# Optimization experiments

Hardware: AMD Instinct MI355X
Metric: run time of the kernel (lower is better)

The kernel has to match this reference:

```python
import jax, jax.numpy as jnp
import numpy as np

VIEW, SEQ, HID = 8, 2048, 1024
ATT = HID // VIEW  # 128


def setup_inputs() -> dict:
    key = jax.random.key(0)
    ks = jax.random.split(key, 12)
    std = 0.02
    return {
        "q": jax.random.normal(ks[0], (VIEW, SEQ, HID), jnp.float32),
        "k": jax.random.normal(ks[1], (VIEW, SEQ, HID), jnp.float32),
        "v": jax.random.normal(ks[2], (VIEW, SEQ, HID), jnp.float32),
        "attn_bias": jax.random.normal(ks[3], (VIEW, SEQ, SEQ), jnp.float32) * std,
        "wq": jax.random.normal(ks[4], (HID, ATT), jnp.float32) * std,
        "bq": jnp.zeros((ATT,), jnp.float32),
        "wk": jax.random.normal(ks[5], (HID, ATT), jnp.float32) * std,
        "bk": jnp.zeros((ATT,), jnp.float32),
        "wv": jax.random.normal(ks[6], (HID, ATT), jnp.float32) * std,
        "bv": jnp.zeros((ATT,), jnp.float32),
        "wo": jax.random.normal(ks[7], (VIEW * ATT, HID), jnp.float32) * std,
        "bo": jnp.zeros((HID,), jnp.float32),
    }


def reference(q, k, v, attn_bias, wq, bq, wk, bk, wv, bv, wo, bo):
    att = wq.shape[1]
    scale = att ** (-0.5)
    qh = (q @ wq + bq) * scale            # [V, S, A]
    kh = k @ wk + bk                      # [V, S, A]
    vh = v @ wv + bv                      # [V, S, A]
    scores = jnp.einsum("vqa,vka->vqk", qh, kh)   # [V, S, S]
    attn = jax.nn.softmax(scores, axis=2)
    # NOTE: source adds the bias AFTER softmax; dropout p=0 (identity).
    attn = attn + attn_bias
    x = jnp.einsum("vqk,vka->vqa", attn, vh)      # [V, S, A]
    vdim, sdim, adim = x.shape
    x = jnp.transpose(x, (1, 0, 2)).reshape(sdim, vdim * adim)  # [S, V*A]
    return x @ wo + bo                    # [S, HID]
```

## Files before the change

kernel.cpp:

```cpp
#include <hip/hip_runtime.h>
#include <math.h>

#define VIEWS 8
#define SEQ 2048
#define HID 1024
#define ATT 128
#define QSCALE 0.08838834764831845f

typedef __attribute__((ext_vector_type(8))) short short8;
typedef __attribute__((ext_vector_type(4))) float f32x4;

__device__ __forceinline__ unsigned short f2bf(float f) {
  union { float f; unsigned u; } a; a.f = f;
  unsigned r = a.u + 0x7FFF + ((a.u >> 16) & 1);
  return (unsigned short)(r >> 16);
}

__global__ __launch_bounds__(256)
void transpose_cvt_f32_bf16(const float* __restrict__ in,
                            unsigned short* __restrict__ out, int R, int C) {
  __shared__ alignas(16) unsigned short T[64][72];
  const int tid = threadIdx.x;
  const int r0 = blockIdx.y * 64, c0 = blockIdx.x * 64;
  const int tr = tid >> 2, tc = (tid & 3) * 16;
#pragma unroll
  for (int u = 0; u < 4; ++u) {
    float4 t = *(const float4*)&in[(size_t)(r0 + tr) * C + c0 + tc + u * 4];
    T[tc + u * 4 + 0][tr] = f2bf(t.x);
    T[tc + u * 4 + 1][tr] = f2bf(t.y);
    T[tc + u * 4 + 2][tr] = f2bf(t.z);
    T[tc + u * 4 + 3][tr] = f2bf(t.w);
  }
  __syncthreads();
  const int oc = tid >> 2, orr = (tid & 3) * 16;
#pragma unroll
  for (int u = 0; u < 2; ++u)
    *(short8*)&out[(size_t)(c0 + oc) * R + r0 + orr + u * 8] =
        *(const short8*)&T[oc][orr + u * 8];
}

__global__ __launch_bounds__(256)
void transpose_qkvw(const float* __restrict__ wq, const float* __restrict__ wk,
                    const float* __restrict__ wv, unsigned short* __restrict__ oq,
                    unsigned short* __restrict__ ok, unsigned short* __restrict__ ov) {
  __shared__ alignas(16) unsigned short T[64][72];
  const int z = blockIdx.z;
  const float* in = (z == 0) ? wq : (z == 1) ? wk : wv;
  unsigned short* out = (z == 0) ? oq : (z == 1) ? ok : ov;
  const int R = HID, C = ATT;
  const int tid = threadIdx.x;
  const int r0 = blockIdx.y * 64, c0 = blockIdx.x * 64;
  const int tr = tid >> 2, tc = (tid & 3) * 16;
#pragma unroll
  for (int u = 0; u < 4; ++u) {
    float4 t = *(const float4*)&in[(size_t)(r0 + tr) * C + c0 + tc + u * 4];
    T[tc + u * 4 + 0][tr] = f2bf(t.x);
    T[tc + u * 4 + 1][tr] = f2bf(t.y);
    T[tc + u * 4 + 2][tr] = f2bf(t.z);
    T[tc + u * 4 + 3][tr] = f2bf(t.w);
  }
  __syncthreads();
  const int oc = tid >> 2, orr = (tid & 3) * 16;
#pragma unroll
  for (int u = 0; u < 2; ++u)
    *(short8*)&out[(size_t)(c0 + oc) * R + r0 + orr + u * 8] =
        *(const short8*)&T[oc][orr + u * 8];
}

__global__ __launch_bounds__(256)
void qkv_proj(const float* __restrict__ q, const float* __restrict__ k,
              const float* __restrict__ v, const unsigned short* __restrict__ wqT,
              const unsigned short* __restrict__ wkT,
              const unsigned short* __restrict__ wvT,
              const float* __restrict__ bq, const float* __restrict__ bk,
              const float* __restrict__ bv, unsigned short* __restrict__ qh,
              unsigned short* __restrict__ kh, unsigned short* __restrict__ vhT) {
  __shared__ alignas(16) unsigned short As[64][72];
  __shared__ alignas(16) unsigned short Bs[128][72];
  const int z = blockIdx.z;
  const float* A = (z == 0) ? q : (z == 1) ? k : v;
  const unsigned short* B = (z == 0) ? wqT : (z == 1) ? wkT : wvT;
  const float* bias = (z == 0) ? bq : (z == 1) ? bk : bv;
  const float scale = (z == 0) ? QSCALE : 1.0f;
  const int tid = threadIdx.x;
  const int m0 = blockIdx.x * 64;
  const int w = tid >> 6, lane = tid & 63;
  const int l16 = lane & 15, quad = lane >> 4;
  const int ar = tid >> 2, ac = (tid & 3) * 16;
  const int br = tid >> 1, bc = (tid & 1) * 32;

  f32x4 acc[8];
#pragma unroll
  for (int i = 0; i < 8; ++i) acc[i] = (f32x4)0.f;

  for (int k0 = 0; k0 < HID; k0 += 64) {
    __syncthreads();
    {
      const float* src = &A[(size_t)(m0 + ar) * HID + k0 + ac];
      unsigned short tmp[16];
#pragma unroll
      for (int u = 0; u < 4; ++u) {
        float4 t = *(const float4*)&src[u * 4];
        tmp[u * 4 + 0] = f2bf(t.x); tmp[u * 4 + 1] = f2bf(t.y);
        tmp[u * 4 + 2] = f2bf(t.z); tmp[u * 4 + 3] = f2bf(t.w);
      }
      *(short8*)&As[ar][ac]     = *(short8*)&tmp[0];
      *(short8*)&As[ar][ac + 8] = *(short8*)&tmp[8];
    }
    {
      const unsigned short* src = &B[(size_t)br * HID + k0 + bc];
#pragma unroll
      for (int u = 0; u < 4; ++u)
        *(short8*)&Bs[br][bc + u * 8] = *(const short8*)&src[u * 8];
    }
    __syncthreads();
#pragma unroll
    for (int ks = 0; ks < 2; ++ks) {
      short8 af = *(const short8*)&As[w * 16 + l16][ks * 32 + quad * 8];
#pragma unroll
      for (int nt = 0; nt < 8; ++nt) {
        short8 bf = *(const short8*)&Bs[nt * 16 + l16][ks * 32 + quad * 8];
        acc[nt] = __builtin_amdgcn_mfma_f32_16x16x32_bf16(af, bf, acc[nt], 0, 0, 0);
      }
    }
  }
  if (z < 2) {
    unsigned short* outp = (z == 0) ? qh : kh;
#pragma unroll
    for (int nt = 0; nt < 8; ++nt) {
      const int col = nt * 16 + l16;
      const float bvv = bias[col];
#pragma unroll
      for (int reg = 0; reg < 4; ++reg) {
        const int row = m0 + w * 16 + quad * 4 + reg;
        outp[(size_t)row * ATT + col] = f2bf((acc[nt][reg] + bvv) * scale);
      }
    }
  } else {
    const int gr = m0 + w * 16 + quad * 4;
    const int vi = gr >> 11, s = gr & (SEQ - 1);
#pragma unroll
    for (int nt = 0; nt < 8; ++nt) {
      const int col = nt * 16 + l16;
      const float bvv = bias[col];
      ushort4 pk;
      pk.x = f2bf(acc[nt][0] + bvv);
      pk.y = f2bf(acc[nt][1] + bvv);
      pk.z = f2bf(acc[nt][2] + bvv);
      pk.w = f2bf(acc[nt][3] + bvv);
      *(ushort4*)&vhT[((size_t)vi * ATT + col) * SEQ + s] = pk;
    }
  }
}

__global__ __launch_bounds__(256, 1)
void flash_fused(const unsigned short* __restrict__ qh,
                 const unsigned short* __restrict__ kh,
                 const unsigned short* __restrict__ vhT,
                 const float* __restrict__ ab,
                 unsigned short* __restrict__ xbf) {
  __shared__ alignas(16) unsigned short Qs[64][136];
  __shared__ alignas(16) unsigned short Ks[2][64][136];
  __shared__ alignas(16) unsigned short VTs[2][128][72];
  __shared__ alignas(16) unsigned short Ps[64][72];
  const int tid = threadIdx.x;
  const int vi = blockIdx.x;
  const int q0 = blockIdx.y * 64;
  const int w = tid >> 6, lane = tid & 63;
  const int l16 = lane & 15, quad = lane >> 4;
  const int wb = w * 16;

  const int kr_ = tid >> 2, kc_ = (tid & 3) * 32;
  const int vr_ = tid >> 1, vc_ = (tid & 1) * 32;
  const unsigned short* kbase = &kh[((size_t)vi * SEQ + kr_) * ATT + kc_];
  const unsigned short* vbase = &vhT[((size_t)vi * ATT + vr_) * SEQ + vc_];

  {
    const int r = tid >> 2, c = (tid & 3) * 32;
    const unsigned short* src = &qh[((size_t)vi * SEQ + q0 + r) * ATT + c];
#pragma unroll
    for (int u = 0; u < 4; ++u)
      *(short8*)&Qs[r][c + u * 8] = *(const short8*)&src[u * 8];
  }

  short8 krg[4], vrg[4];
#pragma unroll
  for (int u = 0; u < 4; ++u) krg[u] = *(const short8*)&kbase[u * 8];
#pragma unroll
  for (int u = 0; u < 4; ++u) vrg[u] = *(const short8*)&vbase[u * 8];

  __syncthreads();
  short8 aF[4];
#pragma unroll
  for (int ks = 0; ks < 4; ++ks)
    aF[ks] = *(const short8*)&Qs[wb + l16][ks * 32 + quad * 8];

  float l_r[4] = {0.f, 0.f, 0.f, 0.f};
  f32x4 o[8], o2[8];
#pragma unroll
  for (int i = 0; i < 8; ++i) { o[i] = (f32x4)0.f; o2[i] = (f32x4)0.f; }

  const float* abrow = &ab[((size_t)vi * SEQ + q0 + wb + l16) * SEQ];

  for (int t = 0; t < SEQ / 64; ++t) {
    const int kt = t * 64;
    const int cur = t & 1;
    float4 abv[4];
    abv[0] = *(const float4*)&abrow[kt + quad * 8];
    abv[1] = *(const float4*)&abrow[kt + quad * 8 + 4];
    abv[2] = *(const float4*)&abrow[kt + 32 + quad * 8];
    abv[3] = *(const float4*)&abrow[kt + 32 + quad * 8 + 4];
#pragma unroll
    for (int u = 0; u < 4; ++u)
      *(short8*)&Ks[cur][kr_][kc_ + u * 8] = krg[u];
#pragma unroll
    for (int u = 0; u < 4; ++u)
      *(short8*)&VTs[cur][vr_][vc_ + u * 8] = vrg[u];
    __syncthreads();
    if (t + 1 < SEQ / 64) {
      const unsigned short* kp = kbase + (size_t)(kt + 64) * ATT;
      const unsigned short* vp = vbase + (kt + 64);
#pragma unroll
      for (int u = 0; u < 4; ++u) krg[u] = *(const short8*)&kp[u * 8];
#pragma unroll
      for (int u = 0; u < 4; ++u) vrg[u] = *(const short8*)&vp[u * 8];
    }
    f32x4 sc[4];
#pragma unroll
    for (int i = 0; i < 4; ++i) sc[i] = (f32x4)0.f;
#pragma unroll
    for (int nt = 0; nt < 4; ++nt) {
#pragma unroll
      for (int ks = 0; ks < 4; ++ks) {
        short8 bF = *(const short8*)&Ks[cur][nt * 16 + l16][ks * 32 + quad * 8];
        sc[nt] = __builtin_amdgcn_mfma_f32_16x16x32_bf16(aF[ks], bF, sc[nt], 0, 0, 0);
      }
    }
#pragma unroll
    for (int nt = 0; nt < 4; ++nt) {
#pragma unroll
      for (int reg = 0; reg < 4; ++reg) {
        float p = __expf(sc[nt][reg]);
        l_r[reg] += p;
        Ps[wb + quad * 4 + reg][nt * 16 + l16] = f2bf(p);
      }
    }
#pragma unroll
    for (int ks = 0; ks < 2; ++ks) {
      short8 pF = *(const short8*)&Ps[wb + l16][ks * 32 + quad * 8];
      short8 bB;
      {
        const float4 u0 = abv[ks * 2], u1 = abv[ks * 2 + 1];
        bB[0] = (short)f2bf(u0.x); bB[1] = (short)f2bf(u0.y);
        bB[2] = (short)f2bf(u0.z); bB[3] = (short)f2bf(u0.w);
        bB[4] = (short)f2bf(u1.x); bB[5] = (short)f2bf(u1.y);
        bB[6] = (short)f2bf(u1.z); bB[7] = (short)f2bf(u1.w);
      }
#pragma unroll
      for (int at = 0; at < 8; ++at) {
        short8 vF = *(const short8*)&VTs[cur][at * 16 + l16][ks * 32 + quad * 8];
        o[at]  = __builtin_amdgcn_mfma_f32_16x16x32_bf16(pF, vF, o[at], 0, 0, 0);
        o2[at] = __builtin_amdgcn_mfma_f32_16x16x32_bf16(bB, vF, o2[at], 0, 0, 0);
      }
    }
  }
  float inv_l[4];
#pragma unroll
  for (int reg = 0; reg < 4; ++reg) {
    float l = l_r[reg];
    l += __shfl_xor(l, 1, 64);
    l += __shfl_xor(l, 2, 64);
    l += __shfl_xor(l, 4, 64);
    l += __shfl_xor(l, 8, 64);
    inv_l[reg] = 1.0f / l;
  }
#pragma unroll
  for (int at = 0; at < 8; ++at) {
    const int col = vi * ATT + at * 16 + l16;
#pragma unroll
    for (int reg = 0; reg < 4; ++reg) {
      const int row = q0 + wb + quad * 4 + reg;
      xbf[(size_t)row * HID + col] = f2bf(o[at][reg] * inv_l[reg] + o2[at][reg]);
    }
  }
}

__global__ __launch_bounds__(256)
void outproj_gemm(const unsigned short* __restrict__ A,
                  const unsigned short* __restrict__ B,
                  const float* __restrict__ bias, float* __restrict__ out) {
  __shared__ alignas(16) unsigned short As[2][64][72];
  __shared__ alignas(16) unsigned short Bs[2][128][72];
  const int tid = threadIdx.x;
  const int m0 = blockIdx.x * 64;
  const int n0 = blockIdx.y * 128;
  const int w = tid >> 6, lane = tid & 63;
  const int l16 = lane & 15, quad = lane >> 4;
  const int ar = tid >> 2, ac = (tid & 3) * 16;
  const int br = tid >> 1, bc = (tid & 1) * 32;
  const unsigned short* abase = &A[(size_t)(m0 + ar) * HID + ac];
  const unsigned short* bbase = &B[(size_t)(n0 + br) * HID + bc];

  f32x4 acc[8];
#pragma unroll
  for (int i = 0; i < 8; ++i) acc[i] = (f32x4)0.f;

  short8 arg0, arg1, brg[4];
  arg0 = *(const short8*)&abase[0];
  arg1 = *(const short8*)&abase[8];
#pragma unroll
  for (int u = 0; u < 4; ++u) brg[u] = *(const short8*)&bbase[u * 8];

  for (int kk = 0; kk < HID / 64; ++kk) {
    const int cur = kk & 1;
    *(short8*)&As[cur][ar][ac]     = arg0;
    *(short8*)&As[cur][ar][ac + 8] = arg1;
#pragma unroll
    for (int u = 0; u < 4; ++u)
      *(short8*)&Bs[cur][br][bc + u * 8] = brg[u];
    __syncthreads();
    if (kk + 1 < HID / 64) {
      const unsigned short* ap = abase + (kk + 1) * 64;
      const unsigned short* bp = bbase + (kk + 1) * 64;
      arg0 = *(const short8*)&ap[0];
      arg1 = *(const short8*)&ap[8];
#pragma unroll
      for (int u = 0; u < 4; ++u) brg[u] = *(const short8*)&bp[u * 8];
    }
#pragma unroll
    for (int ks = 0; ks < 2; ++ks) {
      short8 af = *(const short8*)&As[cur][w * 16 + l16][ks * 32 + quad * 8];
#pragma unroll
      for (int nt = 0; nt < 8; ++nt) {
        short8 bf = *(const short8*)&Bs[cur][nt * 16 + l16][ks * 32 + quad * 8];
        acc[nt] = __builtin_amdgcn_mfma_f32_16x16x32_bf16(af, bf, acc[nt], 0, 0, 0);
      }
    }
  }
#pragma unroll
  for (int nt = 0; nt < 8; ++nt) {
    const int col = n0 + nt * 16 + l16;
    const float bvv = bias[col];
#pragma unroll
    for (int reg = 0; reg < 4; ++reg) {
      const int row = m0 + w * 16 + quad * 4 + reg;
      out[(size_t)row * HID + col] = acc[nt][reg] + bvv;
    }
  }
}

extern "C" void kernel_launch(void* const* d_in, const int* in_sizes, int n_in,
                              void* d_out, int out_size, void* d_ws, size_t ws_size,
                              hipStream_t stream) {
  const float* q   = (const float*)d_in[0];
  const float* k   = (const float*)d_in[1];
  const float* v   = (const float*)d_in[2];
  const float* ab  = (const float*)d_in[3];
  const float* wq  = (const float*)d_in[4];
  const float* bq  = (const float*)d_in[5];
  const float* wk  = (const float*)d_in[6];
  const float* bk  = (const float*)d_in[7];
  const float* wv  = (const float*)d_in[8];
  const float* bv  = (const float*)d_in[9];
  const float* wo  = (const float*)d_in[10];
  const float* bo  = (const float*)d_in[11];
  float* out = (float*)d_out;

  char* ws = (char*)d_ws;
  const size_t PROJ_B = (size_t)VIEWS * SEQ * ATT * 2;
  unsigned short* qh  = (unsigned short*)(ws);
  unsigned short* kh  = (unsigned short*)(ws + PROJ_B);
  unsigned short* vhT = (unsigned short*)(ws + 2 * PROJ_B);
  unsigned short* xbf = (unsigned short*)(ws + 3 * PROJ_B);
  char* wbase = ws + 4 * PROJ_B;
  unsigned short* wqT = (unsigned short*)(wbase);
  unsigned short* wkT = (unsigned short*)(wbase + 262144);
  unsigned short* wvT = (unsigned short*)(wbase + 2 * 262144);
  unsigned short* woT = (unsigned short*)(wbase + 3 * 262144);

  dim3 blk(256);
  transpose_qkvw<<<dim3(2, 16, 3), blk, 0, stream>>>(wq, wk, wv, wqT, wkT, wvT);
  transpose_cvt_f32_bf16<<<dim3(16, 16), blk, 0, stream>>>(wo, woT, HID, HID);
  qkv_proj<<<dim3(256, 1, 3), blk, 0, stream>>>(q, k, v, wqT, wkT, wvT,
                                                bq, bk, bv, qh, kh, vhT);
  flash_fused<<<dim3(VIEWS, SEQ / 64), blk, 0, stream>>>(qh, kh, vhT, ab, xbf);
  outproj_gemm<<<dim3(SEQ / 64, HID / 128), blk, 0, stream>>>(xbf, woT, bo, out);
}
```

Before: 416.7 us.

## Load QKV projection operands directly into MFMA fragments, dropping LDS staging

Rewrites qkv_proj so each wave loads its A rows (fp32, converted to bf16 in registers) and B weight rows straight from global memory into MFMA fragments, removing the shared-memory tiles and both barriers per k-step. Block tile shrinks to 32 rows with waves split 2x2 over M and N, the grid doubles to 512 blocks per projection, and launch bounds request 4 blocks per CU. This trades LDS traffic and sync stalls for redundant global/L2 loads: each A row is now read by two waves and each weight row by many blocks, and the per-lane global access pattern is strided.

```diff
diff --git a/kernel.cpp b/kernel.cpp
--- a/kernel.cpp
+++ b/kernel.cpp
@@ -67,7 +67,7 @@
         *(const short8*)&T[oc][orr + u * 8];
 }
 
-__global__ __launch_bounds__(256)
+__global__ __launch_bounds__(256, 4)
 void qkv_proj(const float* __restrict__ q, const float* __restrict__ k,
               const float* __restrict__ v, const unsigned short* __restrict__ wqT,
               const unsigned short* __restrict__ wkT,
@@ -75,73 +75,70 @@
               const float* __restrict__ bq, const float* __restrict__ bk,
               const float* __restrict__ bv, unsigned short* __restrict__ qh,
               unsigned short* __restrict__ kh, unsigned short* __restrict__ vhT) {
-  __shared__ alignas(16) unsigned short As[64][72];
-  __shared__ alignas(16) unsigned short Bs[128][72];
   const int z = blockIdx.z;
   const float* A = (z == 0) ? q : (z == 1) ? k : v;
   const unsigned short* B = (z == 0) ? wqT : (z == 1) ? wkT : wvT;
   const float* bias = (z == 0) ? bq : (z == 1) ? bk : bv;
   const float scale = (z == 0) ? QSCALE : 1.0f;
   const int tid = threadIdx.x;
-  const int m0 = blockIdx.x * 64;
   const int w = tid >> 6, lane = tid & 63;
   const int l16 = lane & 15, quad = lane >> 4;
-  const int ar = tid >> 2, ac = (tid & 3) * 16;
-  const int br = tid >> 1, bc = (tid & 1) * 32;
-
-  f32x4 acc[8];
-#pragma unroll
-  for (int i = 0; i < 8; ++i) acc[i] = (f32x4)0.f;
-
+  const int mbase = blockIdx.x * 32 + (w & 1) * 16;
+  const int n0 = (w >> 1) * 64;
+
+  const float* arow = &A[(size_t)(mbase + l16) * HID + quad * 8];
+  const unsigned short* bbase = &B[(size_t)(n0 + l16) * HID + quad * 8];
+
+  f32x4 acc[4];
+#pragma unroll
+  for (int i = 0; i < 4; ++i) acc[i] = (f32x4)0.f;
+
+#pragma unroll 2
   for (int k0 = 0; k0 < HID; k0 += 64) {
-    __syncthreads();
-    {
-      const float* src = &A[(size_t)(m0 + ar) * HID + k0 + ac];
-      unsigned short tmp[16];
-#pragma unroll
-      for (int u = 0; u < 4; ++u) {
-        float4 t = *(const float4*)&src[u * 4];
-        tmp[u * 4 + 0] = f2bf(t.x); tmp[u * 4 + 1] = f2bf(t.y);
-        tmp[u * 4 + 2] = f2bf(t.z); tmp[u * 4 + 3] = f2bf(t.w);
-      }
-      *(short8*)&As[ar][ac]     = *(short8*)&tmp[0];
-      *(short8*)&As[ar][ac + 8] = *(short8*)&tmp[8];
-    }
-    {
-      const unsigned short* src = &B[(size_t)br * HID + k0 + bc];
-#pragma unroll
-      for (int u = 0; u < 4; ++u)
-        *(short8*)&Bs[br][bc + u * 8] = *(const short8*)&src[u * 8];
-    }
-    __syncthreads();
-#pragma unroll
-    for (int ks = 0; ks < 2; ++ks) {
-      short8 af = *(const short8*)&As[w * 16 + l16][ks * 32 + quad * 8];
-#pragma unroll
-      for (int nt = 0; nt < 8; ++nt) {
-        short8 bf = *(const short8*)&Bs[nt * 16 + l16][ks * 32 + quad * 8];
-        acc[nt] = __builtin_amdgcn_mfma_f32_16x16x32_bf16(af, bf, acc[nt], 0, 0, 0);
-      }
-    }
-  }
+    const float4 a0 = *(const float4*)&arow[k0];
+    const float4 a1 = *(const float4*)&arow[k0 + 4];
+    const float4 a2 = *(const float4*)&arow[k0 + 32];
+    const float4 a3 = *(const float4*)&arow[k0 + 36];
+    short8 bfr[8];
+#pragma unroll
+    for (int nt = 0; nt < 4; ++nt) {
+      bfr[nt * 2]     = *(const short8*)&bbase[(size_t)nt * 16 * HID + k0];
+      bfr[nt * 2 + 1] = *(const short8*)&bbase[(size_t)nt * 16 * HID + k0 + 32];
+    }
+    short8 af0, af1;
+    af0[0] = (short)f2bf(a0.x); af0[1] = (short)f2bf(a0.y);
+    af0[2] = (short)f2bf(a0.z); af0[3] = (short)f2bf(a0.w);
+    af0[4] = (short)f2bf(a1.x); af0[5] = (short)f2bf(a1.y);
+    af0[6] = (short)f2bf(a1.z); af0[7] = (short)f2bf(a1.w);
+    af1[0] = (short)f2bf(a2.x); af1[1] = (short)f2bf(a2.y);
+    af1[2] = (short)f2bf(a2.z); af1[3] = (short)f2bf(a2.w);
+    af1[4] = (short)f2bf(a3.x); af1[5] = (short)f2bf(a3.y);
+    af1[6] = (short)f2bf(a3.z); af1[7] = (short)f2bf(a3.w);
+#pragma unroll
+    for (int nt = 0; nt < 4; ++nt) {
+      acc[nt] = __builtin_amdgcn_mfma_f32_16x16x32_bf16(af0, bfr[nt * 2],     acc[nt], 0, 0, 0);
+      acc[nt] = __builtin_amdgcn_mfma_f32_16x16x32_bf16(af1, bfr[nt * 2 + 1], acc[nt], 0, 0, 0);
+    }
+  }
+
   if (z < 2) {
     unsigned short* outp = (z == 0) ? qh : kh;
 #pragma unroll
-    for (int nt = 0; nt < 8; ++nt) {
-      const int col = nt * 16 + l16;
+    for (int nt = 0; nt < 4; ++nt) {
+      const int col = n0 + nt * 16 + l16;
       const float bvv = bias[col];
 #pragma unroll
       for (int reg = 0; reg < 4; ++reg) {
-        const int row = m0 + w * 16 + quad * 4 + reg;
+        const int row = mbase + quad * 4 + reg;
         outp[(size_t)row * ATT + col] = f2bf((acc[nt][reg] + bvv) * scale);
       }
     }
   } else {
-    const int gr = m0 + w * 16 + quad * 4;
+    const int gr = mbase + quad * 4;
     const int vi = gr >> 11, s = gr & (SEQ - 1);
 #pragma unroll
-    for (int nt = 0; nt < 8; ++nt) {
-      const int col = nt * 16 + l16;
+    for (int nt = 0; nt < 4; ++nt) {
+      const int col = n0 + nt * 16 + l16;
       const float bvv = bias[col];
       ushort4 pk;
       pk.x = f2bf(acc[nt][0] + bvv);
@@ -381,7 +378,7 @@
   dim3 blk(256);
   transpose_qkvw<<<dim3(2, 16, 3), blk, 0, stream>>>(wq, wk, wv, wqT, wkT, wvT);
   transpose_cvt_f32_bf16<<<dim3(16, 16), blk, 0, stream>>>(wo, woT, HID, HID);
-  qkv_proj<<<dim3(256, 1, 3), blk, 0, stream>>>(q, k, v, wqT, wkT, wvT,
+  qkv_proj<<<dim3(512, 1, 3), blk, 0, stream>>>(q, k, v, wqT, wkT, wvT,
                                                 bq, bk, bv, qh, kh, vhT);
   flash_fused<<<dim3(VIEWS, SEQ / 64), blk, 0, stream>>>(qh, kh, vhT, ab, xbf);
   outproj_gemm<<<dim3(SEQ / 64, HID / 128), blk, 0, stream>>>(xbf, woT, bo, out);
```

Result: slower. 486.0 us (+16.6%).
